# Kernel optimization log

Measured on AMD Instinct MI355X. Metric: run time of the kernel, lower is better.

Reference implementation:

```python
import jax, jax.numpy as jnp
import numpy as np

B, P, N, E, IN, HID, NL, MULT = 4, 8, 2000, 2000, 16, 128, 3, 4
LOGIT_CLIP = 10.0

def setup_inputs() -> dict:
    key = jax.random.key(0)
    ks = jax.random.split(key, 8)
    s = 0.05
    return {
        "node_features": jax.random.normal(ks[0], (B, P, N, IN), jnp.float32),
        "incidence": jax.random.uniform(ks[1], (B, N, E), jnp.float32),  # weighted incidence
        "W_in": s * jax.random.normal(ks[2], (IN, HID), jnp.float32),
        "edge_Ws": s * jax.random.normal(ks[3], (NL, HID, HID), jnp.float32),
        "node_Ws": s * jax.random.normal(ks[4], (NL, HID, HID), jnp.float32),
        "W1": s * jax.random.normal(ks[5], (HID, MULT * HID), jnp.float32),
        "W2": s * jax.random.normal(ks[6], (MULT * HID, HID), jnp.float32),
        "W_dec": s * jax.random.normal(ks[7], (HID, 1), jnp.float32),
    }

def reference(node_features, incidence, W_in, edge_Ws, node_Ws, W1, W2, W_dec):
    # node_features: [B,P,N,in]; incidence H: [B,N,E] (broadcast over P instead of torch's repeat)
    x = node_features @ W_in                                   # [B,P,N,h]
    H = incidence
    n_layers = edge_Ws.shape[0]
    for l in range(n_layers):
        # node -> hyperedge aggregation: H^T @ x
        e = jnp.einsum('bne,bpnd->bped', H, x)                 # [B,P,E,h]
        e = jax.nn.relu(e @ edge_Ws[l])
        # hyperedge -> node aggregation: H @ e
        x = jnp.einsum('bne,bped->bpnd', H, e)                 # [B,P,N,h]
        x = jax.nn.relu(x @ node_Ws[l])
    # MLP: Linear -> ReLU -> Linear (dropout = 0)
    h = jax.nn.relu(x @ W1) @ W2                               # [B,P,N,h]
    out = h @ W_dec                                            # [B,P,N,1]
    out = out / jnp.sqrt(jnp.asarray(W_in.shape[1], jnp.float32))
    out = LOGIT_CLIP * jnp.tanh(out)
    return out
```

## Files before the change

### kernel.cpp

```cpp
#include <hip/hip_runtime.h>
#include <hip/hip_bf16.h>


typedef __attribute__((ext_vector_type(8))) short bf16x8;
typedef __attribute__((ext_vector_type(4))) float f32x4;

#define GLL16(gp, lp) __builtin_amdgcn_global_load_lds(                      \
    (const __attribute__((address_space(1))) void*)(gp),                     \
    (__attribute__((address_space(3))) void*)(lp), 16, 0, 0)

__device__ __forceinline__ unsigned short f2bf(float v) {
  __hip_bfloat16 h = __float2bfloat16(v);
  return __builtin_bit_cast(unsigned short, h);
}
__device__ __forceinline__ float bf2f(unsigned short u) {
  unsigned int x = ((unsigned int)u) << 16;
  return __builtin_bit_cast(float, x);
}

__global__ void convH_k(const float* __restrict__ H,
                        unsigned short* __restrict__ Hb,
                        unsigned short* __restrict__ HTb) {
  int b  = blockIdx.z;
  int n0 = blockIdx.y * 32, e0 = blockIdx.x * 32;
  __shared__ float t[32][33];
  int tx = threadIdx.x & 31, ty = threadIdx.x >> 5;
  for (int r = ty; r < 32; r += 8) {
    int n = n0 + r, e = e0 + tx;
    float v = (n < 2000 && e < 2000) ? H[((long)b * 2000 + n) * 2000 + e] : 0.f;
    t[r][tx] = v;
    Hb[((long)b * 2048 + n) * 2048 + e] = f2bf(v);
  }
  __syncthreads();
  for (int r = ty; r < 32; r += 8) {
    HTb[((long)b * 2048 + (e0 + r)) * 2048 + (n0 + tx)] = f2bf(t[tx][r]);
  }
}

__global__ void transposeW_k(const float* __restrict__ src,
                             unsigned short* __restrict__ dst, int R, int C) {
  __shared__ float t[32][33];
  int c0 = blockIdx.x * 32, r0 = blockIdx.y * 32;
  int tx = threadIdx.x & 31, ty = threadIdx.x >> 5;
  for (int rr = ty; rr < 32; rr += 8) {
    int rI = r0 + rr, cI = c0 + tx;
    t[rr][tx] = (rI < R && cI < C) ? src[(long)rI * C + cI] : 0.f;
  }
  __syncthreads();
  for (int rr = ty; rr < 32; rr += 8) {
    int cO = c0 + rr, rO = r0 + tx;
    if (cO < C && rO < R) dst[(long)cO * R + rO] = f2bf(t[tx][rr]);
  }
}

__global__ __launch_bounds__(256) void x0_k(
    const float* __restrict__ nf, const float* __restrict__ Win,
    unsigned short* __restrict__ xTb) {
  __shared__ float nfs[128][16];
  __shared__ float wins[2048];

  int bp = blockIdx.y;
  int n0 = blockIdx.x * 128;
  int tid = threadIdx.x;

  {
    int r = tid >> 1, c = (tid & 1) * 8;
    int n = n0 + r;
    float4 v0 = make_float4(0.f, 0.f, 0.f, 0.f), v1 = v0;
    if (n < 2000) {
      const float* src = nf + ((long)bp * 2000 + n) * 16 + c;
      v0 = *(const float4*)src;
      v1 = *(const float4*)(src + 4);
    }
    *(float4*)&nfs[r][c]     = v0;
    *(float4*)&nfs[r][c + 4] = v1;
  }
  {
    int base = tid * 8;
    float4 a = *(const float4*)(Win + base);
    float4 b = *(const float4*)(Win + base + 4);
    *(float4*)&wins[base]     = a;
    *(float4*)&wins[base + 4] = b;
  }
  __syncthreads();

  int d = tid & 127, half = tid >> 7;
  float wcol[16];
#pragma unroll
  for (int k = 0; k < 16; k++) wcol[k] = wins[k * 128 + d];

  unsigned short* dst = xTb + ((long)bp * 128 + d) * 2048 + n0 + half * 64;
#pragma unroll
  for (int oct = 0; oct < 8; oct++) {
    bf16x8 pk;
#pragma unroll
    for (int j = 0; j < 8; j++) {
      int nl = half * 64 + oct * 8 + j;
      float v = 0.f;
#pragma unroll
      for (int k = 0; k < 16; k++) v += nfs[nl][k] * wcol[k];
      pk[j] = (short)f2bf(v);
    }
    *(bf16x8*)(dst + oct * 8) = pk;
  }
}

__global__ void wfuse_k(const float* __restrict__ W2, const float* __restrict__ Wdec,
                        float* __restrict__ wf) {
  int i = blockIdx.x * 256 + threadIdx.x;
  if (i < 512) {
    float s = 0.f;
#pragma unroll 8
    for (int j = 0; j < 128; j++) s += W2[i * 128 + j] * Wdec[j];
    wf[i] = s;
  }
}

template <int WN, int WT>
__global__ __launch_bounds__(256, 2) void gemm_fused(
    const unsigned short* __restrict__ A, int lda, long strideA,
    const unsigned short* __restrict__ BT, long strideBT,
    const unsigned short* __restrict__ Wt,
    unsigned short* __restrict__ Cn, int ldc, long strideCn,
    unsigned short* __restrict__ Ct, int ldct, long strideCt, int K) {
  int wgid = blockIdx.x;
  int orig = (wgid & 7) * 32 + (wgid >> 3);
  int mblk = orig & 15;
  int rest = orig >> 4;
  int ntl  = rest & 3;
  int b    = rest >> 2;
  int m0   = mblk * 128;
  int bp0  = b * 8 + ntl * 2;
  A += (long)b * strideA;
  const unsigned short* BTb = BT + (long)bp0 * strideBT;

  __shared__ unsigned short smem[32768];

  int tid  = threadIdx.x;
  int lane = tid & 63;
  int w    = tid >> 6;
  int wr   = w >> 1, wc = w & 1;
  int fr   = lane & 15;
  int fg   = lane >> 4;

  const unsigned short* Agp[2];
  const unsigned short* Bgp[4];
#pragma unroll
  for (int i = 0; i < 2; i++) {
    int s = i * 256 + tid, row = s >> 2, gc = (s & 3) ^ ((row >> 1) & 3);
    Agp[i] = A + (long)(m0 + row) * lda + gc * 8;
  }
#pragma unroll
  for (int i = 0; i < 4; i++) {
    int s = i * 256 + tid, row = s >> 2, gc = (s & 3) ^ ((row >> 1) & 3);
    Bgp[i] = BTb + (long)row * 2048 + gc * 8;
  }

#define STAGE(sel, tk) do {                                                  \
    int _k = (tk) * 32;                                                      \
    _Pragma("unroll")                                                        \
    for (int i = 0; i < 2; i++)                                              \
      GLL16(Agp[i] + _k, smem + (sel) * 12288 + (i * 256 + tid) * 8);        \
    _Pragma("unroll")                                                        \
    for (int i = 0; i < 4; i++)                                              \
      GLL16(Bgp[i] + _k, smem + (sel) * 12288 + 4096 + (i * 256 + tid) * 8); \
  } while (0)

  f32x4 acc[4][8] = {};
  const int cIdx = (fg ^ ((fr >> 1) & 3)) * 8;

#define COMPUTE(sel) do {                                                    \
    const unsigned short* As_ = smem + (sel) * 12288;                        \
    const unsigned short* Bs_ = As_ + 4096;                                  \
    bf16x8 af[4], bv[8];                                                     \
    _Pragma("unroll")                                                        \
    for (int m = 0; m < 4; m++)                                              \
      af[m] = *(const bf16x8*)&As_[(wr * 64 + m * 16 + fr) * 32 + cIdx];     \
    _Pragma("unroll")                                                        \
    for (int n = 0; n < 8; n++)                                              \
      bv[n] = *(const bf16x8*)&Bs_[(wc * 128 + n * 16 + fr) * 32 + cIdx];    \
    __builtin_amdgcn_s_setprio(1);                                           \
    _Pragma("unroll")                                                        \
    for (int m = 0; m < 4; m++)                                              \
      _Pragma("unroll")                                                      \
      for (int n = 0; n < 8; n++)                                            \
        acc[m][n] = __builtin_amdgcn_mfma_f32_16x16x32_bf16(af[m], bv[n],    \
                                                            acc[m][n], 0, 0, 0); \
    __builtin_amdgcn_s_setprio(0);                                           \
  } while (0)

#define VMW(n) asm volatile("s_waitcnt vmcnt(" #n ")" ::: "memory")
#define BARR __builtin_amdgcn_s_barrier()
#define SCH0 __builtin_amdgcn_sched_barrier(0)

  int nt = K >> 5;

  STAGE(0, 0);
  int t = 0;
  for (; t + 2 < nt; t += 2) {
    STAGE(1, t + 1);
    VMW(6); BARR; SCH0;
    COMPUTE(0);
    BARR;
    STAGE(0, t + 2);
    VMW(6); BARR; SCH0;
    COMPUTE(1);
    BARR;
  }
  STAGE(1, nt - 1);
  VMW(6); BARR; SCH0;
  COMPUTE(0);
  BARR;
  VMW(0); BARR; SCH0;
  COMPUTE(1);
#undef STAGE
#undef COMPUTE
  __syncthreads();

  unsigned short* Gs = smem;
#pragma unroll
  for (int m = 0; m < 4; m++) {
#pragma unroll
    for (int n = 0; n < 8; n++) {
      int rowb = wr * 64 + m * 16 + fg * 4;
      int col  = wc * 128 + n * 16 + fr;
      int ch = col >> 3, ci = col & 7;
#pragma unroll
      for (int r = 0; r < 4; r++) {
        int row = rowb + r;
        Gs[row * 256 + ((ch ^ (row & 7)) * 8) + ci] = f2bf(acc[m][n][r]);
      }
    }
  }
  __syncthreads();

  f32x4 acc2[4][8] = {};
#pragma unroll
  for (int kk = 0; kk < 4; kk++) {
    bf16x8 a2[4], b2[8];
#pragma unroll
    for (int m = 0; m < 4; m++) {
      int row = wr * 64 + m * 16 + fr;
      int ch = wc * 16 + kk * 4 + fg;
      a2[m] = *(const bf16x8*)&Gs[row * 256 + ((ch ^ (row & 7)) * 8)];
    }
#pragma unroll
    for (int n = 0; n < 8; n++) {
      int row = n * 16 + fr;
      b2[n] = *(const bf16x8*)&Wt[row * 128 + (kk * 4 + fg) * 8];
    }
#pragma unroll
    for (int m = 0; m < 4; m++)
#pragma unroll
      for (int n = 0; n < 8; n++)
        acc2[m][n] = __builtin_amdgcn_mfma_f32_16x16x32_bf16(a2[m], b2[n], acc2[m][n], 0, 0, 0);
  }

  if (WN) {
#pragma unroll
    for (int m = 0; m < 4; m++) {
#pragma unroll
      for (int n = 0; n < 8; n++) {
        int rowb = m0 + wr * 64 + m * 16 + fg * 4;
        int col  = n * 16 + fr;
        unsigned short* p = Cn + (bp0 + wc) * strideCn + (long)rowb * ldc + col;
        p[0]       = f2bf(fmaxf(acc2[m][n][0], 0.f));
        p[ldc]     = f2bf(fmaxf(acc2[m][n][1], 0.f));
        p[2 * ldc] = f2bf(fmaxf(acc2[m][n][2], 0.f));
        p[3 * ldc] = f2bf(fmaxf(acc2[m][n][3], 0.f));
      }
    }
  }

  if (WT) {
    __syncthreads();
    unsigned short* GsT = smem;
#pragma unroll
    for (int m = 0; m < 4; m++) {
#pragma unroll
      for (int n = 0; n < 8; n++) {
        int rowb = wr * 64 + m * 16 + fg * 4;
        int col  = n * 16 + fr;
        int slot = (rowb >> 3) ^ (col & 7);
        ushort4 pk;
        pk.x = f2bf(fmaxf(acc2[m][n][0], 0.f));
        pk.y = f2bf(fmaxf(acc2[m][n][1], 0.f));
        pk.z = f2bf(fmaxf(acc2[m][n][2], 0.f));
        pk.w = f2bf(fmaxf(acc2[m][n][3], 0.f));
        *(ushort4*)&GsT[wc * 16384 + col * 128 + slot * 8 + (rowb & 7)] = pk;
      }
    }
    __syncthreads();
#pragma unroll
    for (int i = 0; i < 16; i++) {
      int s = i * 256 + tid;
      int pI = s >> 11, col = (s >> 4) & 127, slot = s & 15;
      int l = slot ^ (col & 7);
      bf16x8 v = *(const bf16x8*)&GsT[pI * 16384 + col * 128 + slot * 8];
      *(bf16x8*)(Ct + (bp0 + pI) * strideCt + (long)col * ldct + m0 + l * 8) = v;
    }
  }
}

__global__ __launch_bounds__(256) void mlp_k(
    const unsigned short* __restrict__ X,
    const unsigned short* __restrict__ W1T,
    const float* __restrict__ wf,
    float* __restrict__ out) {
  __shared__ unsigned short Xs[128 * 128];
  __shared__ unsigned short Bs[128 * 128];
  __shared__ float rowacc[128];

  int tid  = threadIdx.x;
  int lane = tid & 63;
  int w    = tid >> 6, wr = w >> 1, wc = w & 1;
  int fr   = lane & 15, fg = lane >> 4;
  long m0  = (long)blockIdx.x * 128;

#pragma unroll
  for (int i = 0; i < 8; i++) {
    int s = i * 256 + tid;
    int r = s >> 4, c = (s & 15) ^ (r & 7);
    GLL16(X + (m0 + r) * 128 + c * 8, (unsigned short*)Xs + s * 8);
  }
  if (tid < 128) rowacc[tid] = 0.f;

  float rs[4][4] = {};

  for (int nb = 0; nb < 4; nb++) {
#pragma unroll
    for (int i = 0; i < 8; i++) {
      int s = i * 256 + tid;
      int r = s >> 4, c = (s & 15) ^ (r & 7);
      GLL16(W1T + (long)(nb * 128 + r) * 128 + c * 8, (unsigned short*)Bs + s * 8);
    }
    __syncthreads();

    f32x4 acc[4][4] = {};
#pragma unroll
    for (int kk = 0; kk < 4; kk++) {
      bf16x8 a2[4], b2[4];
#pragma unroll
      for (int m = 0; m < 4; m++) {
        int row = wr * 64 + m * 16 + fr;
        int c = kk * 4 + fg;
        a2[m] = *(const bf16x8*)&Xs[row * 128 + ((c ^ (row & 7)) * 8)];
      }
#pragma unroll
      for (int n = 0; n < 4; n++) {
        int row = wc * 64 + n * 16 + fr;
        int c = kk * 4 + fg;
        b2[n] = *(const bf16x8*)&Bs[row * 128 + ((c ^ (row & 7)) * 8)];
      }
#pragma unroll
      for (int m = 0; m < 4; m++)
#pragma unroll
        for (int n = 0; n < 4; n++)
          acc[m][n] = __builtin_amdgcn_mfma_f32_16x16x32_bf16(a2[m], b2[n], acc[m][n], 0, 0, 0);
    }

#pragma unroll
    for (int n = 0; n < 4; n++) {
      float wv = wf[nb * 128 + wc * 64 + n * 16 + fr];
#pragma unroll
      for (int m = 0; m < 4; m++)
#pragma unroll
        for (int r = 0; r < 4; r++)
          rs[m][r] += fmaxf(acc[m][n][r], 0.f) * wv;
    }
    __syncthreads();
  }

#pragma unroll
  for (int m = 0; m < 4; m++)
#pragma unroll
    for (int r = 0; r < 4; r++) {
      float v = rs[m][r];
      v += __shfl_xor(v, 1, 64);
      v += __shfl_xor(v, 2, 64);
      v += __shfl_xor(v, 4, 64);
      v += __shfl_xor(v, 8, 64);
      if (fr == 0) atomicAdd(&rowacc[wr * 64 + m * 16 + fg * 4 + r], v);
    }
  __syncthreads();

  if (tid < 128) {
    long row = m0 + tid;
    int bp = (int)(row >> 11), n = (int)(row & 2047);
    if (n < 2000)
      out[(long)bp * 2000 + n] = 10.f * tanhf(rowacc[tid] * 0.08838834764831843f);
  }
}

extern "C" void kernel_launch(void* const* d_in, const int* in_sizes, int n_in,
                              void* d_out, int out_size, void* d_ws, size_t ws_size,
                              hipStream_t stream) {
  const float* nf    = (const float*)d_in[0];
  const float* H     = (const float*)d_in[1];
  const float* Win   = (const float*)d_in[2];
  const float* edgeW = (const float*)d_in[3];
  const float* nodeW = (const float*)d_in[4];
  const float* W1    = (const float*)d_in[5];
  const float* W2    = (const float*)d_in[6];
  const float* Wdec  = (const float*)d_in[7];
  float* out = (float*)d_out;

  char* ws = (char*)d_ws;
  unsigned short* Hb   = (unsigned short*)(ws + 0);
  unsigned short* HTb  = (unsigned short*)(ws + 33554432);
  unsigned short* xb   = (unsigned short*)(ws + 67108864);
  unsigned short* xTb  = (unsigned short*)(ws + 83886080);
  unsigned short* eTb  = (unsigned short*)(ws + 100663296);
  unsigned short* edgeWT = (unsigned short*)(ws + 117440512);
  unsigned short* nodeWT = (unsigned short*)(ws + 117538816);
  unsigned short* W1T    = (unsigned short*)(ws + 117637120);
  float*          wf     = (float*)(ws + 117768192);
  (void)ws_size; (void)in_sizes; (void)n_in; (void)out_size;

  convH_k<<<dim3(64, 64, 4), 256, 0, stream>>>(H, Hb, HTb);
  for (int l = 0; l < 3; l++) {
    transposeW_k<<<dim3(4, 4), 256, 0, stream>>>(edgeW + l * 16384, edgeWT + l * 16384, 128, 128);
    transposeW_k<<<dim3(4, 4), 256, 0, stream>>>(nodeW + l * 16384, nodeWT + l * 16384, 128, 128);
  }
  transposeW_k<<<dim3(16, 4), 256, 0, stream>>>(W1, W1T, 128, 512);
  wfuse_k<<<2, 256, 0, stream>>>(W2, Wdec, wf);
  x0_k<<<dim3(16, 32), 256, 0, stream>>>(nf, Win, xTb);

  for (int l = 0; l < 3; l++) {
    gemm_fused<0, 1><<<dim3(256), 256, 0, stream>>>(
        HTb, 2048, 2048L * 2048, xTb, 128L * 2048,
        edgeWT + l * 16384,
        nullptr, 0, 0, eTb, 2048, 128L * 2048, 2048);
    if (l < 2) {
      gemm_fused<0, 1><<<dim3(256), 256, 0, stream>>>(
          Hb, 2048, 2048L * 2048, eTb, 128L * 2048,
          nodeWT + l * 16384,
          nullptr, 0, 0, xTb, 2048, 128L * 2048, 2048);
    } else {
      gemm_fused<1, 1><<<dim3(256), 256, 0, stream>>>(
          Hb, 2048, 2048L * 2048, eTb, 128L * 2048,
          nodeWT + l * 16384,
          xb, 128, 2048L * 128, xTb, 2048, 128L * 2048, 2048);
    }
  }

  mlp_k<<<dim3(512), 256, 0, stream>>>(xb, W1T, wf, out);
}
```

Before: 364.7 us.

## Shrink fused GEMM tiles to 64x128 per block and quadruple the grid

The fused aggregation-plus-weight GEMM now gives each 128-thread block one (batch, partition) slice and 64 rows, instead of 256-thread blocks covering 128 rows across two partitions. The grid grows from 256 to 1024 blocks and each block uses less shared memory, so more waves are resident per compute unit to hide memory and MFMA latency on a 256-CU device. In exchange, each incidence tile is now reused for only one partition rather than two, which raises global traffic for the A operand. Per-block synchronisation overhead also grows relative to the work done.

Measured after the change: 460.8 us. +26.3%, slower.

```diff
diff --git a/kernel.cpp b/kernel.cpp
--- a/kernel.cpp
+++ b/kernel.cpp
@@ -117,29 +117,25 @@
 }
 
 template <int WN, int WT>
-__global__ __launch_bounds__(256, 2) void gemm_fused(
-    const unsigned short* __restrict__ A, int lda, long strideA,
-    const unsigned short* __restrict__ BT, long strideBT,
+__global__ __launch_bounds__(128, 2) void gemm_fused(
+    const unsigned short* __restrict__ A, int lda, long strideA, int aDiv,
+    const unsigned short* __restrict__ BT, int ldbt, long strideBT,
     const unsigned short* __restrict__ Wt,
     unsigned short* __restrict__ Cn, int ldc, long strideCn,
     unsigned short* __restrict__ Ct, int ldct, long strideCt, int K) {
   int wgid = blockIdx.x;
-  int orig = (wgid & 7) * 32 + (wgid >> 3);
-  int mblk = orig & 15;
-  int rest = orig >> 4;
-  int ntl  = rest & 3;
-  int b    = rest >> 2;
-  int m0   = mblk * 128;
-  int bp0  = b * 8 + ntl * 2;
-  A += (long)b * strideA;
-  const unsigned short* BTb = BT + (long)bp0 * strideBT;
-
-  __shared__ unsigned short smem[32768];
+  int orig = (wgid & 7) * 128 + (wgid >> 3);
+  int mblk = orig & 31;
+  int bz   = orig >> 5;
+  A  += (long)(bz / aDiv) * strideA;
+  BT += (long)bz * strideBT;
+  int m0 = mblk * 64;
+
+  __shared__ unsigned short smem[12288];
 
   int tid  = threadIdx.x;
   int lane = tid & 63;
   int w    = tid >> 6;
-  int wr   = w >> 1, wc = w & 1;
   int fr   = lane & 15;
   int fg   = lane >> 4;
 
@@ -147,43 +143,43 @@
   const unsigned short* Bgp[4];
 #pragma unroll
   for (int i = 0; i < 2; i++) {
-    int s = i * 256 + tid, row = s >> 2, gc = (s & 3) ^ ((row >> 1) & 3);
+    int s = i * 128 + tid, row = s >> 2, gc = (s & 3) ^ ((row >> 1) & 3);
     Agp[i] = A + (long)(m0 + row) * lda + gc * 8;
   }
 #pragma unroll
   for (int i = 0; i < 4; i++) {
-    int s = i * 256 + tid, row = s >> 2, gc = (s & 3) ^ ((row >> 1) & 3);
-    Bgp[i] = BTb + (long)row * 2048 + gc * 8;
+    int s = i * 128 + tid, row = s >> 2, gc = (s & 3) ^ ((row >> 1) & 3);
+    Bgp[i] = BT + (long)row * ldbt + gc * 8;
   }
 
 #define STAGE(sel, tk) do {                                                  \
     int _k = (tk) * 32;                                                      \
     _Pragma("unroll")                                                        \
     for (int i = 0; i < 2; i++)                                              \
-      GLL16(Agp[i] + _k, smem + (sel) * 12288 + (i * 256 + tid) * 8);        \
+      GLL16(Agp[i] + _k, smem + (sel) * 6144 + (i * 128 + tid) * 8);         \
     _Pragma("unroll")                                                        \
     for (int i = 0; i < 4; i++)                                              \
-      GLL16(Bgp[i] + _k, smem + (sel) * 12288 + 4096 + (i * 256 + tid) * 8); \
+      GLL16(Bgp[i] + _k, smem + (sel) * 6144 + 2048 + (i * 128 + tid) * 8);  \
   } while (0)
 
-  f32x4 acc[4][8] = {};
+  f32x4 acc[4][4] = {};
   const int cIdx = (fg ^ ((fr >> 1) & 3)) * 8;
 
 #define COMPUTE(sel) do {                                                    \
-    const unsigned short* As_ = smem + (sel) * 12288;                        \
-    const unsigned short* Bs_ = As_ + 4096;                                  \
-    bf16x8 af[4], bv[8];                                                     \
+    const unsigned short* As_ = smem + (sel) * 6144;                         \
+    const unsigned short* Bs_ = As_ + 2048;                                  \
+    bf16x8 af[4], bv[4];                                                     \
     _Pragma("unroll")                                                        \
     for (int m = 0; m < 4; m++)                                              \
-      af[m] = *(const bf16x8*)&As_[(wr * 64 + m * 16 + fr) * 32 + cIdx];     \
+      af[m] = *(const bf16x8*)&As_[(m * 16 + fr) * 32 + cIdx];               \
     _Pragma("unroll")                                                        \
-    for (int n = 0; n < 8; n++)                                              \
-      bv[n] = *(const bf16x8*)&Bs_[(wc * 128 + n * 16 + fr) * 32 + cIdx];    \
+    for (int n = 0; n < 4; n++)                                              \
+      bv[n] = *(const bf16x8*)&Bs_[(w * 64 + n * 16 + fr) * 32 + cIdx];      \
     __builtin_amdgcn_s_setprio(1);                                           \
     _Pragma("unroll")                                                        \
     for (int m = 0; m < 4; m++)                                              \
       _Pragma("unroll")                                                      \
-      for (int n = 0; n < 8; n++)                                            \
+      for (int n = 0; n < 4; n++)                                            \
         acc[m][n] = __builtin_amdgcn_mfma_f32_16x16x32_bf16(af[m], bv[n],    \
                                                             acc[m][n], 0, 0, 0); \
     __builtin_amdgcn_s_setprio(0);                                           \
@@ -221,38 +217,38 @@
 #pragma unroll
   for (int m = 0; m < 4; m++) {
 #pragma unroll
-    for (int n = 0; n < 8; n++) {
-      int rowb = wr * 64 + m * 16 + fg * 4;
-      int col  = wc * 128 + n * 16 + fr;
+    for (int n = 0; n < 4; n++) {
+      int rowb = m * 16 + fg * 4;
+      int col  = w * 64 + n * 16 + fr;
       int ch = col >> 3, ci = col & 7;
 #pragma unroll
       for (int r = 0; r < 4; r++) {
         int row = rowb + r;
-        Gs[row * 256 + ((ch ^ (row & 7)) * 8) + ci] = f2bf(acc[m][n][r]);
+        Gs[row * 128 + ((ch ^ (row & 7)) * 8) + ci] = f2bf(acc[m][n][r]);
       }
     }
   }
   __syncthreads();
 
-  f32x4 acc2[4][8] = {};
+  f32x4 acc2[4][4] = {};
 #pragma unroll
   for (int kk = 0; kk < 4; kk++) {
-    bf16x8 a2[4], b2[8];
+    bf16x8 a2[4], b2[4];
 #pragma unroll
     for (int m = 0; m < 4; m++) {
-      int row = wr * 64 + m * 16 + fr;
-      int ch = wc * 16 + kk * 4 + fg;
-      a2[m] = *(const bf16x8*)&Gs[row * 256 + ((ch ^ (row & 7)) * 8)];
-    }
-#pragma unroll
-    for (int n = 0; n < 8; n++) {
-      int row = n * 16 + fr;
+      int row = m * 16 + fr;
+      int c = kk * 4 + fg;
+      a2[m] = *(const bf16x8*)&Gs[row * 128 + ((c ^ (fr & 7)) * 8)];
+    }
+#pragma unroll
+    for (int n = 0; n < 4; n++) {
+      int row = w * 64 + n * 16 + fr;
       b2[n] = *(const bf16x8*)&Wt[row * 128 + (kk * 4 + fg) * 8];
     }
 #pragma unroll
     for (int m = 0; m < 4; m++)
 #pragma unroll
-      for (int n = 0; n < 8; n++)
+      for (int n = 0; n < 4; n++)
         acc2[m][n] = __builtin_amdgcn_mfma_f32_16x16x32_bf16(a2[m], b2[n], acc2[m][n], 0, 0, 0);
   }
 
@@ -260,10 +256,10 @@
 #pragma unroll
     for (int m = 0; m < 4; m++) {
 #pragma unroll
-      for (int n = 0; n < 8; n++) {
-        int rowb = m0 + wr * 64 + m * 16 + fg * 4;
-        int col  = n * 16 + fr;
-        unsigned short* p = Cn + (bp0 + wc) * strideCn + (long)rowb * ldc + col;
+      for (int n = 0; n < 4; n++) {
+        int rowb = m0 + m * 16 + fg * 4;
+        int col  = w * 64 + n * 16 + fr;
+        unsigned short* p = Cn + bz * strideCn + (long)rowb * ldc + col;
         p[0]       = f2bf(fmaxf(acc2[m][n][0], 0.f));
         p[ldc]     = f2bf(fmaxf(acc2[m][n][1], 0.f));
         p[2 * ldc] = f2bf(fmaxf(acc2[m][n][2], 0.f));
@@ -278,26 +274,26 @@
 #pragma unroll
     for (int m = 0; m < 4; m++) {
 #pragma unroll
-      for (int n = 0; n < 8; n++) {
-        int rowb = wr * 64 + m * 16 + fg * 4;
-        int col  = n * 16 + fr;
+      for (int n = 0; n < 4; n++) {
+        int rowb = m * 16 + fg * 4;
+        int col  = w * 64 + n * 16 + fr;
         int slot = (rowb >> 3) ^ (col & 7);
         ushort4 pk;
         pk.x = f2bf(fmaxf(acc2[m][n][0], 0.f));
         pk.y = f2bf(fmaxf(acc2[m][n][1], 0.f));
         pk.z = f2bf(fmaxf(acc2[m][n][2], 0.f));
         pk.w = f2bf(fmaxf(acc2[m][n][3], 0.f));
-        *(ushort4*)&GsT[wc * 16384 + col * 128 + slot * 8 + (rowb & 7)] = pk;
+        *(ushort4*)&GsT[col * 64 + slot * 8 + (rowb & 7)] = pk;
       }
     }
     __syncthreads();
-#pragma unroll
-    for (int i = 0; i < 16; i++) {
-      int s = i * 256 + tid;
-      int pI = s >> 11, col = (s >> 4) & 127, slot = s & 15;
-      int l = slot ^ (col & 7);
-      bf16x8 v = *(const bf16x8*)&GsT[pI * 16384 + col * 128 + slot * 8];
-      *(bf16x8*)(Ct + (bp0 + pI) * strideCt + (long)col * ldct + m0 + l * 8) = v;
+    unsigned short* CtB = Ct + bz * strideCt + m0;
+    int col = tid;
+#pragma unroll
+    for (int s = 0; s < 8; s++) {
+      int l = s ^ (col & 7);
+      bf16x8 v = *(const bf16x8*)&GsT[col * 64 + s * 8];
+      *(bf16x8*)(CtB + (long)col * ldct + l * 8) = v;
     }
   }
 }
@@ -427,18 +423,18 @@
   x0_k<<<dim3(16, 32), 256, 0, stream>>>(nf, Win, xTb);
 
   for (int l = 0; l < 3; l++) {
-    gemm_fused<0, 1><<<dim3(256), 256, 0, stream>>>(
-        HTb, 2048, 2048L * 2048, xTb, 128L * 2048,
+    gemm_fused<0, 1><<<dim3(1024), 128, 0, stream>>>(
+        HTb, 2048, 2048L * 2048, 8, xTb, 2048, 128L * 2048,
         edgeWT + l * 16384,
         nullptr, 0, 0, eTb, 2048, 128L * 2048, 2048);
     if (l < 2) {
-      gemm_fused<0, 1><<<dim3(256), 256, 0, stream>>>(
-          Hb, 2048, 2048L * 2048, eTb, 128L * 2048,
+      gemm_fused<0, 1><<<dim3(1024), 128, 0, stream>>>(
+          Hb, 2048, 2048L * 2048, 8, eTb, 2048, 128L * 2048,
           nodeWT + l * 16384,
           nullptr, 0, 0, xTb, 2048, 128L * 2048, 2048);
     } else {
-      gemm_fused<1, 1><<<dim3(256), 256, 0, stream>>>(
-          Hb, 2048, 2048L * 2048, eTb, 128L * 2048,
+      gemm_fused<1, 1><<<dim3(1024), 128, 0, stream>>>(
+          Hb, 2048, 2048L * 2048, 8, eTb, 2048, 128L * 2048,
           nodeWT + l * 16384,
           xb, 128, 2048L * 128, xTb, 2048, 128L * 2048, 2048);
     }
```
